# Performance work log

Measured on AMD Instinct MI355X. Metric: run time of the kernel, lower is better.

The kernel has to match this reference:

```python
import jax, jax.numpy as jnp
import numpy as np

N, E, IN_DIM, HID, OUT, H = 50000, 800000, 128, 96, 96, 4
C1, C2 = HID // H, OUT // H
EPS = 1e-5

def _lin(key, out_f, in_f):
    kw, kb = jax.random.split(key)
    s = 1.0 / np.sqrt(in_f)
    W = jax.random.uniform(kw, (out_f, in_f), jnp.float32, -s, s)
    b = jax.random.uniform(kb, (out_f,), jnp.float32, -s, s)
    return W, b

def setup_inputs() -> dict:
    key = jax.random.key(0)
    ks = jax.random.split(key, 16)
    x = jax.random.normal(ks[0], (N, IN_DIM), jnp.float32)
    edge_index = jax.random.randint(ks[1], (2, E), 0, N, jnp.int64)
    Wq1, bq1 = _lin(ks[2], HID, IN_DIM)
    Wk1, bk1 = _lin(ks[3], HID, IN_DIM)
    Wv1, bv1 = _lin(ks[4], HID, IN_DIM)
    Ws1, bs1 = _lin(ks[5], HID, IN_DIM)
    Wb1 = _lin(ks[6], 1, 3 * HID)[0]
    Wq2, bq2 = _lin(ks[7], OUT, HID)
    Wk2, bk2 = _lin(ks[8], OUT, HID)
    Wv2, bv2 = _lin(ks[9], OUT, HID)
    Ws2, bs2 = _lin(ks[10], OUT, HID)
    Wb2 = _lin(ks[11], 1, 3 * OUT)[0]
    gamma = jnp.ones((OUT,), jnp.float32)
    beta = jnp.zeros((OUT,), jnp.float32)
    return dict(x=x, edge_index=edge_index, Wq1=Wq1, bq1=bq1, Wk1=Wk1, bk1=bk1,
                Wv1=Wv1, bv1=bv1, Ws1=Ws1, bs1=bs1, Wb1=Wb1,
                Wq2=Wq2, bq2=bq2, Wk2=Wk2, bk2=bk2, Wv2=Wv2, bv2=bv2,
                Ws2=Ws2, bs2=bs2, Wb2=Wb2, gamma=gamma, beta=beta)

def transformer_conv(x, src, dst, Wq, bq, Wk, bk, Wv, bv, Ws, bs, Wb, heads, ch):
    n = x.shape[0]
    q = (x @ Wq.T + bq).reshape(n, heads, ch)
    k = (x @ Wk.T + bk).reshape(n, heads, ch)
    v = (x @ Wv.T + bv).reshape(n, heads, ch)
    # per-edge attention logits [E, H]
    alpha = jnp.einsum('ehc,ehc->eh', q[dst], k[src]) / jnp.sqrt(jnp.float32(ch))
    amax = jax.ops.segment_max(alpha, dst, num_segments=n)
    a = jnp.exp(alpha - amax[dst])
    denom = jax.ops.segment_sum(a, dst, num_segments=n)
    a = a / denom[dst]
    msg = v[src] * a[:, :, None]                       # [E, H, C]
    out = jax.ops.segment_sum(msg, dst, num_segments=n).reshape(n, heads * ch)
    x_r = x @ Ws.T + bs                                # root/skip transform
    g = jax.nn.sigmoid(jnp.concatenate([out, x_r, out - x_r], -1) @ Wb.T)
    return g * x_r + (1.0 - g) * out

def reference(x, edge_index, Wq1, bq1, Wk1, bk1, Wv1, bv1, Ws1, bs1, Wb1,
              Wq2, bq2, Wk2, bk2, Wv2, bv2, Ws2, bs2, Wb2, gamma, beta):
    src, dst = edge_index[0], edge_index[1]
    h = transformer_conv(x, src, dst, Wq1, bq1, Wk1, bk1, Wv1, bv1, Ws1, bs1, Wb1, H, C1)
    h = jax.nn.gelu(h, approximate=False)
    h = transformer_conv(h, src, dst, Wq2, bq2, Wk2, bk2, Wv2, bv2, Ws2, bs2, Wb2, H, C2)
    mu = jnp.mean(h, axis=-1, keepdims=True)
    var = jnp.mean(jnp.square(h - mu), axis=-1, keepdims=True)
    return (h - mu) / jnp.sqrt(var + EPS) * gamma + beta
```

## Files before the change

kernel.cpp:

```cpp
#include <hip/hip_runtime.h>
#include <hip/hip_bf16.h>
#include <hip/hip_fp16.h>
#include <math.h>

constexpr int NN = 50000;
constexpr int EE = 800000;
constexpr int SCAN_NB = (NN + 255) / 256;

typedef short v8s __attribute__((ext_vector_type(8)));
typedef float v4f __attribute__((ext_vector_type(4)));

__device__ __forceinline__ short f2b(float f){
  __hip_bfloat16 h = __float2bfloat16(f);
  return *reinterpret_cast<short*>(&h);
}
__device__ __forceinline__ __half2 u2h2(unsigned int u){
  union { unsigned int u; __half2 h; } c; c.u = u; return c.h;
}

__global__ void hist_kernel(const int* __restrict__ ei, int* __restrict__ deg){
  int e = blockIdx.x * blockDim.x + threadIdx.x;
  if (e < EE) atomicAdd(&deg[ei[EE + e]], 1);
}

__global__ __launch_bounds__(256) void partial_sum_kernel(const int* __restrict__ deg,
                                                          int* __restrict__ psum){
  int b = blockIdx.x, tid = threadIdx.x, lane = tid & 63, wv = tid >> 6;
  int i = b * 256 + tid;
  int v = (i < NN) ? deg[i] : 0;
  #pragma unroll
  for (int m = 1; m < 64; m <<= 1) v += __shfl_xor(v, m);
  __shared__ int ws[4];
  if (lane == 0) ws[wv] = v;
  __syncthreads();
  if (tid == 0) psum[b] = ws[0] + ws[1] + ws[2] + ws[3];
}

__global__ __launch_bounds__(256) void scan_partials_kernel(int* __restrict__ psum){
  int tid = threadIdx.x, lane = tid & 63, wv = tid >> 6;
  int own = (tid < SCAN_NB) ? psum[tid] : 0;
  int v = own;
  #pragma unroll
  for (int off = 1; off < 64; off <<= 1){
    int t = __shfl_up(v, off);
    if (lane >= off) v += t;
  }
  __shared__ int ws[4];
  if (lane == 63) ws[wv] = v;
  __syncthreads();
  int add = 0;
  #pragma unroll
  for (int w = 0; w < 4; w++) if (w < wv) add += ws[w];
  if (tid < SCAN_NB) psum[tid] = v + add - own;
}

__global__ __launch_bounds__(256) void final_scan_kernel(const int* __restrict__ deg,
                                                         const int* __restrict__ psum,
                                                         int* __restrict__ row_ptr,
                                                         int* __restrict__ cursor){
  int b = blockIdx.x, tid = threadIdx.x, lane = tid & 63, wv = tid >> 6;
  int i = b * 256 + tid;
  int d = (i < NN) ? deg[i] : 0;
  int v = d;
  #pragma unroll
  for (int off = 1; off < 64; off <<= 1){
    int t = __shfl_up(v, off);
    if (lane >= off) v += t;
  }
  __shared__ int ws[4];
  if (lane == 63) ws[wv] = v;
  __syncthreads();
  int add = psum[b];
  #pragma unroll
  for (int w = 0; w < 4; w++) if (w < wv) add += ws[w];
  if (i < NN){
    row_ptr[i + 1] = add + v;
    cursor[i]      = add + v - d;
  }
  if (i == 0) row_ptr[0] = 0;
}

__global__ void fill_kernel(const int* __restrict__ ei, int* __restrict__ cursor,
                            int* __restrict__ col_src){
  int e = blockIdx.x * blockDim.x + threadIdx.x;
  if (e < EE){
    int src = ei[e], dst = ei[EE + e];
    int pos = atomicAdd(&cursor[dst], 1);
    col_src[pos] = src;
  }
}

__global__ void pack_kernel(const float* __restrict__ Wq, const float* __restrict__ bq,
                            const float* __restrict__ Wk, const float* __restrict__ bk,
                            const float* __restrict__ Wv, const float* __restrict__ bv,
                            const float* __restrict__ Ws, const float* __restrict__ bs,
                            short* __restrict__ Wcat, float* __restrict__ bcat, int K){
  int c = blockIdx.x;
  int which = c / 96, r = c % 96;
  const float* Wsel = which == 0 ? Wq : which == 1 ? Wk : which == 2 ? Wv : Ws;
  const float* bsel = which == 0 ? bq : which == 1 ? bk : which == 2 ? bv : bs;
  for (int k = threadIdx.x; k < K; k += blockDim.x)
    Wcat[(size_t)c * K + k] = f2b(Wsel[(size_t)r * K + k]);
  if (threadIdx.x == 0) bcat[c] = bsel[r];
}

template<int K, bool AF32>
__global__ __launch_bounds__(256) void gemm_kernel(const void* __restrict__ Ain,
                                                   const short* __restrict__ Wcat,
                                                   const float* __restrict__ bcat,
                                                   float* __restrict__ qs,
                                                   __half* __restrict__ kvb,
                                                   int M){
  constexpr int KP = K + 8;
  constexpr int UNITS = K / 8;
  __shared__ __attribute__((aligned(16))) short As[64 * KP];
  __shared__ __attribute__((aligned(16))) short Bs[128 * KP];
  const int tid = threadIdx.x;
  const int rt = blockIdx.x * 64;

  #pragma unroll
  for (int it = 0; it < (64 * UNITS) / 256; ++it){
    int li = it * 256 + tid;
    int row = li / UNITS, u = li % UNITS;
    int grow = min(rt + row, M - 1);
    if constexpr (AF32){
      const float* A = (const float*)Ain;
      float4 a0 = *(const float4*)(A + (size_t)grow * K + u * 8);
      float4 a1 = *(const float4*)(A + (size_t)grow * K + u * 8 + 4);
      v8s o;
      o[0] = f2b(a0.x); o[1] = f2b(a0.y); o[2] = f2b(a0.z); o[3] = f2b(a0.w);
      o[4] = f2b(a1.x); o[5] = f2b(a1.y); o[6] = f2b(a1.z); o[7] = f2b(a1.w);
      *(v8s*)&As[row * KP + u * 8] = o;
    } else {
      const short* A = (const short*)Ain;
      *(v8s*)&As[row * KP + u * 8] = *(const v8s*)(A + (size_t)grow * K + u * 8);
    }
  }

  const int lane = tid & 63;
  const int wid  = tid >> 6;
  const int wm = wid >> 1, wn = wid & 1;
  const int fr = lane & 15, fk = lane >> 4;

  for (int p = 0; p < 3; ++p){
    __syncthreads();
    #pragma unroll
    for (int it = 0; it < (128 * UNITS) / 256; ++it){
      int li = it * 256 + tid;
      int row = li / UNITS, u = li % UNITS;
      int gcol = p * 128 + row;
      *(v8s*)&Bs[row * KP + u * 8] = *(const v8s*)(Wcat + (size_t)gcol * K + u * 8);
    }
    __syncthreads();

    v4f acc[2][4];
    #pragma unroll
    for (int i = 0; i < 2; i++)
      #pragma unroll
      for (int j = 0; j < 4; j++) acc[i][j] = (v4f){0.f, 0.f, 0.f, 0.f};

    #pragma unroll
    for (int ks = 0; ks < K / 32; ++ks){
      const int kofs = ks * 32 + fk * 8;
      v8s a[2], b[4];
      #pragma unroll
      for (int i = 0; i < 2; i++)
        a[i] = *(const v8s*)&As[(wm * 32 + i * 16 + fr) * KP + kofs];
      #pragma unroll
      for (int j = 0; j < 4; j++)
        b[j] = *(const v8s*)&Bs[(wn * 64 + j * 16 + fr) * KP + kofs];
      #pragma unroll
      for (int i = 0; i < 2; i++)
        #pragma unroll
        for (int j = 0; j < 4; j++)
          acc[i][j] = __builtin_amdgcn_mfma_f32_16x16x32_bf16(a[i], b[j], acc[i][j], 0, 0, 0);
    }

    #pragma unroll
    for (int i = 0; i < 2; i++){
      #pragma unroll
      for (int j = 0; j < 4; j++){
        const int gcol = p * 128 + wn * 64 + j * 16 + fr;
        const float bias = bcat[gcol];
        #pragma unroll
        for (int r = 0; r < 4; r++){
          const int grow = rt + wm * 32 + i * 16 + fk * 4 + r;
          if (grow < M){
            float val = acc[i][j][r] + bias;
            if (gcol < 96)       qs[(size_t)grow * 192 + gcol] = val;
            else if (gcol < 192) kvb[(size_t)grow * 192 + (gcol - 96)] = __float2half(val);
            else if (gcol < 288) kvb[(size_t)grow * 192 + 96 + (gcol - 192)] = __float2half(val);
            else                 qs[(size_t)grow * 192 + 96 + (gcol - 288)] = val;
          }
        }
      }
    }
  }
}

__global__ __launch_bounds__(256) void attn_kernel(
    const float* __restrict__ qs, const __half* __restrict__ kv,
    const int* __restrict__ row_ptr, const int* __restrict__ col_src,
    const float* __restrict__ Wb, const float* __restrict__ gamma,
    const float* __restrict__ beta, float* __restrict__ outp,
    short* __restrict__ h1b, int mode){
  const int lane = threadIdx.x & 63;
  const int wid  = threadIdx.x >> 6;
  const int n = blockIdx.x * 4 + wid;
  if (n >= NN) return;
  const int h_a = lane & 3;
  const int g_a = lane >> 2;
  const int l_v = lane & 15;
  const int vg  = lane >> 4;
  const int h_v = l_v >> 2;

  __half2 qh[12];
  {
    const float* qrow = qs + (size_t)n * 192 + h_a * 24;
    #pragma unroll
    for (int i = 0; i < 12; i++)
      qh[i] = __floats2half2_rn(qrow[2 * i], qrow[2 * i + 1]);
  }
  const int rs = row_ptr[n], re = row_ptr[n + 1];
  float m = -INFINITY, s = 0.f;
  float acc[6] = {0.f, 0.f, 0.f, 0.f, 0.f, 0.f};

  for (int cb = rs; cb < re; cb += 16){
    const int cn = re - cb;
    int srcv = col_src[cb + min(g_a, cn - 1)];
    int sb[4];
    #pragma unroll
    for (int st = 0; st < 4; st++)
      sb[st] = __shfl(srcv, 4 * min(st * 4 + vg, cn - 1));
    unsigned int vd[4][3];
    #pragma unroll
    for (int st = 0; st < 4; st++){
      const unsigned int* vp =
        (const unsigned int*)((const char*)kv + (size_t)sb[st] * 384 + 192 + 12 * l_v);
      vd[st][0] = vp[0]; vd[st][1] = vp[1]; vd[st][2] = vp[2];
    }
    const uint4* kp = (const uint4*)((const char*)kv + (size_t)srcv * 384 + h_a * 48);
    uint4 u0 = kp[0], u1 = kp[1], u2 = kp[2];
    __half2 d0 = __floats2half2_rn(0.f, 0.f), d1 = d0;
    d0 = __hfma2(qh[0],  u2h2(u0.x), d0); d1 = __hfma2(qh[1],  u2h2(u0.y), d1);
    d0 = __hfma2(qh[2],  u2h2(u0.z), d0); d1 = __hfma2(qh[3],  u2h2(u0.w), d1);
    d0 = __hfma2(qh[4],  u2h2(u1.x), d0); d1 = __hfma2(qh[5],  u2h2(u1.y), d1);
    d0 = __hfma2(qh[6],  u2h2(u1.z), d0); d1 = __hfma2(qh[7],  u2h2(u1.w), d1);
    d0 = __hfma2(qh[8],  u2h2(u2.x), d0); d1 = __hfma2(qh[9],  u2h2(u2.y), d1);
    d0 = __hfma2(qh[10], u2h2(u2.z), d0); d1 = __hfma2(qh[11], u2h2(u2.w), d1);
    float dot = __low2float(d0) + __high2float(d0) + __low2float(d1) + __high2float(d1);
    float al = (g_a < cn) ? dot * 0.2041241452319315f : -INFINITY;

    float cm = al;
    cm = fmaxf(cm, __shfl_xor(cm, 4));
    cm = fmaxf(cm, __shfl_xor(cm, 8));
    cm = fmaxf(cm, __shfl_xor(cm, 16));
    cm = fmaxf(cm, __shfl_xor(cm, 32));
    float nm = fmaxf(m, cm);
    float r  = __expf(m - nm);
    float e  = __expf(al - nm);
    float cs = e;
    cs += __shfl_xor(cs, 4);
    cs += __shfl_xor(cs, 8);
    cs += __shfl_xor(cs, 16);
    cs += __shfl_xor(cs, 32);
    s = s * r + cs;
    m = nm;

    float rv = __shfl(r, h_v);
    __half2 ch0 = __floats2half2_rn(0.f, 0.f), ch1 = ch0, ch2 = ch0;
    #pragma unroll
    for (int st = 0; st < 4; st++){
      int eidx = st * 4 + vg;
      float w = __shfl(e, 4 * min(eidx, cn - 1) + h_v);
      if (eidx >= cn) w = 0.f;
      __half2 w2 = __float2half2_rn(w);
      ch0 = __hfma2(w2, u2h2(vd[st][0]), ch0);
      ch1 = __hfma2(w2, u2h2(vd[st][1]), ch1);
      ch2 = __hfma2(w2, u2h2(vd[st][2]), ch2);
    }
    acc[0] = fmaf(acc[0], rv, __low2float(ch0));
    acc[1] = fmaf(acc[1], rv, __high2float(ch0));
    acc[2] = fmaf(acc[2], rv, __low2float(ch1));
    acc[3] = fmaf(acc[3], rv, __high2float(ch1));
    acc[4] = fmaf(acc[4], rv, __low2float(ch2));
    acc[5] = fmaf(acc[5], rv, __high2float(ch2));
  }

  #pragma unroll
  for (int i = 0; i < 6; i++){
    acc[i] += __shfl_xor(acc[i], 16);
    acc[i] += __shfl_xor(acc[i], 32);
  }
  float sv  = __shfl(s, h_v);
  float inv = (re > rs) ? 1.0f / sv : 0.f;
  float o[6], xr[6];
  #pragma unroll
  for (int i = 0; i < 6; i++) o[i] = acc[i] * inv;
  const float* xrp = qs + (size_t)n * 192 + 96 + 6 * l_v;
  #pragma unroll
  for (int i = 0; i < 6; i++) xr[i] = xrp[i];

  float p = 0.f;
  #pragma unroll
  for (int i = 0; i < 6; i++){
    int f = 6 * l_v + i;
    p += Wb[f] * o[i] + Wb[96 + f] * xr[i] + Wb[192 + f] * (o[i] - xr[i]);
  }
  p += __shfl_xor(p, 1);
  p += __shfl_xor(p, 2);
  p += __shfl_xor(p, 4);
  p += __shfl_xor(p, 8);
  float g = 1.0f / (1.0f + __expf(-p));
  float y[6];
  #pragma unroll
  for (int i = 0; i < 6; i++) y[i] = g * xr[i] + (1.0f - g) * o[i];

  if (mode == 0){
    #pragma unroll
    for (int i = 0; i < 6; i++)
      y[i] = 0.5f * y[i] * (1.0f + erff(y[i] * 0.7071067811865475f));
    if (vg == 0){
      short* op = h1b + (size_t)n * 96 + 6 * l_v;
      #pragma unroll
      for (int i = 0; i < 6; i++) op[i] = f2b(y[i]);
    }
  } else {
    float ssum = y[0] + y[1] + y[2] + y[3] + y[4] + y[5];
    ssum += __shfl_xor(ssum, 1);
    ssum += __shfl_xor(ssum, 2);
    ssum += __shfl_xor(ssum, 4);
    ssum += __shfl_xor(ssum, 8);
    float mu = ssum * (1.0f / 96.0f);
    float vsum = 0.f;
    #pragma unroll
    for (int i = 0; i < 6; i++){ float d = y[i] - mu; vsum += d * d; }
    vsum += __shfl_xor(vsum, 1);
    vsum += __shfl_xor(vsum, 2);
    vsum += __shfl_xor(vsum, 4);
    vsum += __shfl_xor(vsum, 8);
    float invs = rsqrtf(vsum * (1.0f / 96.0f) + 1e-5f);
    if (vg == 0){
      float* op = outp + (size_t)n * 96 + 6 * l_v;
      #pragma unroll
      for (int i = 0; i < 6; i++){
        int f = 6 * l_v + i;
        op[i] = (y[i] - mu) * invs * gamma[f] + beta[f];
      }
    }
  }
}

extern "C" void kernel_launch(void* const* d_in, const int* in_sizes, int n_in,
                              void* d_out, int out_size, void* d_ws, size_t ws_size,
                              hipStream_t stream){
  const float* x    = (const float*)d_in[0];
  const int*   ei   = (const int*)d_in[1];
  const float* Wq1  = (const float*)d_in[2];
  const float* bq1  = (const float*)d_in[3];
  const float* Wk1  = (const float*)d_in[4];
  const float* bk1  = (const float*)d_in[5];
  const float* Wv1  = (const float*)d_in[6];
  const float* bv1  = (const float*)d_in[7];
  const float* Ws1  = (const float*)d_in[8];
  const float* bs1  = (const float*)d_in[9];
  const float* Wb1  = (const float*)d_in[10];
  const float* Wq2  = (const float*)d_in[11];
  const float* bq2  = (const float*)d_in[12];
  const float* Wk2  = (const float*)d_in[13];
  const float* bk2  = (const float*)d_in[14];
  const float* Wv2  = (const float*)d_in[15];
  const float* bv2  = (const float*)d_in[16];
  const float* Ws2  = (const float*)d_in[17];
  const float* bs2  = (const float*)d_in[18];
  const float* Wb2  = (const float*)d_in[19];
  const float* gamma = (const float*)d_in[20];
  const float* beta  = (const float*)d_in[21];
  float* out = (float*)d_out;

  char* ws = (char*)d_ws;
  size_t off = 0;
  auto take = [&](size_t b) -> void* {
    void* p = ws + off;
    off += (b + 255) & ~(size_t)255;
    return p;
  };
  float* qs            = (float*)take((size_t)NN * 192 * 4);
  __half* kvb          = (__half*)take((size_t)NN * 192 * 2);
  short* h1b           = (short*)take((size_t)NN * 96 * 2);
  short* Wcat          = (short*)take((size_t)384 * 128 * 2);
  float* bcat          = (float*)take(384 * 4);
  int* deg             = (int*)take((size_t)NN * 4);
  int* cursor          = (int*)take((size_t)NN * 4);
  int* row_ptr         = (int*)take((size_t)(NN + 1) * 4);
  int* col_src         = (int*)take((size_t)EE * 4);
  int* psum            = (int*)take((size_t)SCAN_NB * 4);

  hipMemsetAsync(deg, 0, (size_t)NN * 4, stream);
  hist_kernel<<<(EE + 255) / 256, 256, 0, stream>>>(ei, deg);
  partial_sum_kernel<<<SCAN_NB, 256, 0, stream>>>(deg, psum);
  scan_partials_kernel<<<1, 256, 0, stream>>>(psum);
  final_scan_kernel<<<SCAN_NB, 256, 0, stream>>>(deg, psum, row_ptr, cursor);
  fill_kernel<<<(EE + 255) / 256, 256, 0, stream>>>(ei, cursor, col_src);

  const int gemm_grid = (NN + 63) / 64;
  pack_kernel<<<384, 128, 0, stream>>>(Wq1, bq1, Wk1, bk1, Wv1, bv1, Ws1, bs1, Wcat, bcat, 128);
  gemm_kernel<128, true><<<gemm_grid, 256, 0, stream>>>(x, Wcat, bcat, qs, kvb, NN);
  attn_kernel<<<(NN + 3) / 4, 256, 0, stream>>>(qs, kvb, row_ptr, col_src, Wb1,
                                                nullptr, nullptr, nullptr, h1b, 0);
  pack_kernel<<<384, 128, 0, stream>>>(Wq2, bq2, Wk2, bk2, Wv2, bv2, Ws2, bs2, Wcat, bcat, 96);
  gemm_kernel<96, false><<<gemm_grid, 256, 0, stream>>>(h1b, Wcat, bcat, qs, kvb, NN);
  attn_kernel<<<(NN + 3) / 4, 256, 0, stream>>>(qs, kvb, row_ptr, col_src, Wb2,
                                                gamma, beta, out, nullptr, 1);
}
```

Baseline: 283.8 us.

## Read GEMM weights from global memory and halve row tile; merge weight packing

The GEMM kernel no longer stages the weight matrix in shared memory. Each wave now loads B fragments straight from global (L2-resident) memory, and the row tile shrinks from 64 to 32, which doubles the grid and cuts the shared-memory footprint and the syncs inside the loop. The two per-layer pack kernels become a single launch writing into separate weight buffers. The intent is better occupancy and fewer barriers, at the cost of repeated global/L2 reads of the weights and less reuse of each B fragment per block.

```diff
diff --git a/kernel.cpp b/kernel.cpp
--- a/kernel.cpp
+++ b/kernel.cpp
@@ -90,18 +90,37 @@
   }
 }
 
-__global__ void pack_kernel(const float* __restrict__ Wq, const float* __restrict__ bq,
-                            const float* __restrict__ Wk, const float* __restrict__ bk,
-                            const float* __restrict__ Wv, const float* __restrict__ bv,
-                            const float* __restrict__ Ws, const float* __restrict__ bs,
-                            short* __restrict__ Wcat, float* __restrict__ bcat, int K){
+__global__ void pack_kernel(
+    const float* __restrict__ Wq1, const float* __restrict__ bq1,
+    const float* __restrict__ Wk1, const float* __restrict__ bk1,
+    const float* __restrict__ Wv1, const float* __restrict__ bv1,
+    const float* __restrict__ Ws1, const float* __restrict__ bs1,
+    const float* __restrict__ Wq2, const float* __restrict__ bq2,
+    const float* __restrict__ Wk2, const float* __restrict__ bk2,
+    const float* __restrict__ Wv2, const float* __restrict__ bv2,
+    const float* __restrict__ Ws2, const float* __restrict__ bs2,
+    short* __restrict__ Wcat1, float* __restrict__ bcat1,
+    short* __restrict__ Wcat2, float* __restrict__ bcat2){
   int c = blockIdx.x;
-  int which = c / 96, r = c % 96;
-  const float* Wsel = which == 0 ? Wq : which == 1 ? Wk : which == 2 ? Wv : Ws;
-  const float* bsel = which == 0 ? bq : which == 1 ? bk : which == 2 ? bv : bs;
+  int layer = c / 384, cc = c % 384;
+  int which = cc / 96, r = cc % 96;
+  const float* Wsel;
+  const float* bsel;
+  int K;
+  short* Wd;
+  float* bd;
+  if (layer == 0){
+    Wsel = which == 0 ? Wq1 : which == 1 ? Wk1 : which == 2 ? Wv1 : Ws1;
+    bsel = which == 0 ? bq1 : which == 1 ? bk1 : which == 2 ? bv1 : bs1;
+    K = 128; Wd = Wcat1; bd = bcat1;
+  } else {
+    Wsel = which == 0 ? Wq2 : which == 1 ? Wk2 : which == 2 ? Wv2 : Ws2;
+    bsel = which == 0 ? bq2 : which == 1 ? bk2 : which == 2 ? bv2 : bs2;
+    K = 96; Wd = Wcat2; bd = bcat2;
+  }
   for (int k = threadIdx.x; k < K; k += blockDim.x)
-    Wcat[(size_t)c * K + k] = f2b(Wsel[(size_t)r * K + k]);
-  if (threadIdx.x == 0) bcat[c] = bsel[r];
+    Wd[(size_t)cc * K + k] = f2b(Wsel[(size_t)r * K + k]);
+  if (threadIdx.x == 0) bd[cc] = bsel[r];
 }
 
 template<int K, bool AF32>
@@ -113,85 +132,69 @@
                                                    int M){
   constexpr int KP = K + 8;
   constexpr int UNITS = K / 8;
-  __shared__ __attribute__((aligned(16))) short As[64 * KP];
-  __shared__ __attribute__((aligned(16))) short Bs[128 * KP];
+  constexpr int TOT = 32 * UNITS;
+  __shared__ __attribute__((aligned(16))) short As[32 * KP];
   const int tid = threadIdx.x;
-  const int rt = blockIdx.x * 64;
-
-  #pragma unroll
-  for (int it = 0; it < (64 * UNITS) / 256; ++it){
+  const int rt = blockIdx.x * 32;
+
+  #pragma unroll
+  for (int it = 0; it < (TOT + 255) / 256; ++it){
     int li = it * 256 + tid;
-    int row = li / UNITS, u = li % UNITS;
-    int grow = min(rt + row, M - 1);
-    if constexpr (AF32){
-      const float* A = (const float*)Ain;
-      float4 a0 = *(const float4*)(A + (size_t)grow * K + u * 8);
-      float4 a1 = *(const float4*)(A + (size_t)grow * K + u * 8 + 4);
-      v8s o;
-      o[0] = f2b(a0.x); o[1] = f2b(a0.y); o[2] = f2b(a0.z); o[3] = f2b(a0.w);
-      o[4] = f2b(a1.x); o[5] = f2b(a1.y); o[6] = f2b(a1.z); o[7] = f2b(a1.w);
-      *(v8s*)&As[row * KP + u * 8] = o;
-    } else {
-      const short* A = (const short*)Ain;
-      *(v8s*)&As[row * KP + u * 8] = *(const v8s*)(A + (size_t)grow * K + u * 8);
-    }
-  }
+    if (li < TOT){
+      int row = li / UNITS, u = li % UNITS;
+      int grow = min(rt + row, M - 1);
+      if constexpr (AF32){
+        const float* A = (const float*)Ain;
+        float4 a0 = *(const float4*)(A + (size_t)grow * K + u * 8);
+        float4 a1 = *(const float4*)(A + (size_t)grow * K + u * 8 + 4);
+        v8s o;
+        o[0] = f2b(a0.x); o[1] = f2b(a0.y); o[2] = f2b(a0.z); o[3] = f2b(a0.w);
+        o[4] = f2b(a1.x); o[5] = f2b(a1.y); o[6] = f2b(a1.z); o[7] = f2b(a1.w);
+        *(v8s*)&As[row * KP + u * 8] = o;
+      } else {
+        const short* A = (const short*)Ain;
+        *(v8s*)&As[row * KP + u * 8] = *(const v8s*)(A + (size_t)grow * K + u * 8);
+      }
+    }
+  }
+  __syncthreads();
 
   const int lane = tid & 63;
   const int wid  = tid >> 6;
-  const int wm = wid >> 1, wn = wid & 1;
+  const int wm = wid & 1, wn = wid >> 1;
   const int fr = lane & 15, fk = lane >> 4;
 
+  #pragma unroll
   for (int p = 0; p < 3; ++p){
-    __syncthreads();
-    #pragma unroll
-    for (int it = 0; it < (128 * UNITS) / 256; ++it){
-      int li = it * 256 + tid;
-      int row = li / UNITS, u = li % UNITS;
-      int gcol = p * 128 + row;
-      *(v8s*)&Bs[row * KP + u * 8] = *(const v8s*)(Wcat + (size_t)gcol * K + u * 8);
-    }
-    __syncthreads();
-
-    v4f acc[2][4];
-    #pragma unroll
-    for (int i = 0; i < 2; i++)
-      #pragma unroll
-      for (int j = 0; j < 4; j++) acc[i][j] = (v4f){0.f, 0.f, 0.f, 0.f};
+    v4f acc[4];
+    #pragma unroll
+    for (int j = 0; j < 4; j++) acc[j] = (v4f){0.f, 0.f, 0.f, 0.f};
 
     #pragma unroll
     for (int ks = 0; ks < K / 32; ++ks){
       const int kofs = ks * 32 + fk * 8;
-      v8s a[2], b[4];
-      #pragma unroll
-      for (int i = 0; i < 2; i++)
-        a[i] = *(const v8s*)&As[(wm * 32 + i * 16 + fr) * KP + kofs];
-      #pragma unroll
-      for (int j = 0; j < 4; j++)
-        b[j] = *(const v8s*)&Bs[(wn * 64 + j * 16 + fr) * KP + kofs];
-      #pragma unroll
-      for (int i = 0; i < 2; i++)
-        #pragma unroll
-        for (int j = 0; j < 4; j++)
-          acc[i][j] = __builtin_amdgcn_mfma_f32_16x16x32_bf16(a[i], b[j], acc[i][j], 0, 0, 0);
-    }
-
-    #pragma unroll
-    for (int i = 0; i < 2; i++){
+      v8s a = *(const v8s*)&As[(wm * 16 + fr) * KP + kofs];
       #pragma unroll
       for (int j = 0; j < 4; j++){
         const int gcol = p * 128 + wn * 64 + j * 16 + fr;
-        const float bias = bcat[gcol];
-        #pragma unroll
-        for (int r = 0; r < 4; r++){
-          const int grow = rt + wm * 32 + i * 16 + fk * 4 + r;
-          if (grow < M){
-            float val = acc[i][j][r] + bias;
-            if (gcol < 96)       qs[(size_t)grow * 192 + gcol] = val;
-            else if (gcol < 192) kvb[(size_t)grow * 192 + (gcol - 96)] = __float2half(val);
-            else if (gcol < 288) kvb[(size_t)grow * 192 + 96 + (gcol - 192)] = __float2half(val);
-            else                 qs[(size_t)grow * 192 + 96 + (gcol - 288)] = val;
-          }
+        v8s b = *(const v8s*)(Wcat + (size_t)gcol * K + kofs);
+        acc[j] = __builtin_amdgcn_mfma_f32_16x16x32_bf16(a, b, acc[j], 0, 0, 0);
+      }
+    }
+
+    #pragma unroll
+    for (int j = 0; j < 4; j++){
+      const int gcol = p * 128 + wn * 64 + j * 16 + fr;
+      const float bias = bcat[gcol];
+      #pragma unroll
+      for (int r = 0; r < 4; r++){
+        const int grow = rt + wm * 16 + fk * 4 + r;
+        if (grow < M){
+          float val = acc[j][r] + bias;
+          if (gcol < 96)       qs[(size_t)grow * 192 + gcol] = val;
+          else if (gcol < 192) kvb[(size_t)grow * 192 + (gcol - 96)] = __float2half(val);
+          else if (gcol < 288) kvb[(size_t)grow * 192 + 96 + (gcol - 192)] = __float2half(val);
+          else                 qs[(size_t)grow * 192 + 96 + (gcol - 288)] = val;
         }
       }
     }
@@ -388,8 +391,10 @@
   float* qs            = (float*)take((size_t)NN * 192 * 4);
   __half* kvb          = (__half*)take((size_t)NN * 192 * 2);
   short* h1b           = (short*)take((size_t)NN * 96 * 2);
-  short* Wcat          = (short*)take((size_t)384 * 128 * 2);
-  float* bcat          = (float*)take(384 * 4);
+  short* Wcat1         = (short*)take((size_t)384 * 128 * 2);
+  short* Wcat2         = (short*)take((size_t)384 * 96 * 2);
+  float* bcat1         = (float*)take(384 * 4);
+  float* bcat2         = (float*)take(384 * 4);
   int* deg             = (int*)take((size_t)NN * 4);
   int* cursor          = (int*)take((size_t)NN * 4);
   int* row_ptr         = (int*)take((size_t)(NN + 1) * 4);
@@ -403,13 +408,15 @@
   final_scan_kernel<<<SCAN_NB, 256, 0, stream>>>(deg, psum, row_ptr, cursor);
   fill_kernel<<<(EE + 255) / 256, 256, 0, stream>>>(ei, cursor, col_src);
 
-  const int gemm_grid = (NN + 63) / 64;
-  pack_kernel<<<384, 128, 0, stream>>>(Wq1, bq1, Wk1, bk1, Wv1, bv1, Ws1, bs1, Wcat, bcat, 128);
-  gemm_kernel<128, true><<<gemm_grid, 256, 0, stream>>>(x, Wcat, bcat, qs, kvb, NN);
+  pack_kernel<<<768, 128, 0, stream>>>(Wq1, bq1, Wk1, bk1, Wv1, bv1, Ws1, bs1,
+                                       Wq2, bq2, Wk2, bk2, Wv2, bv2, Ws2, bs2,
+                                       Wcat1, bcat1, Wcat2, bcat2);
+
+  const int gemm_grid = (NN + 31) / 32;
+  gemm_kernel<128, true><<<gemm_grid, 256, 0, stream>>>(x, Wcat1, bcat1, qs, kvb, NN);
   attn_kernel<<<(NN + 3) / 4, 256, 0, stream>>>(qs, kvb, row_ptr, col_src, Wb1,
                                                 nullptr, nullptr, nullptr, h1b, 0);
-  pack_kernel<<<384, 128, 0, stream>>>(Wq2, bq2, Wk2, bk2, Wv2, bv2, Ws2, bs2, Wcat, bcat, 96);
-  gemm_kernel<96, false><<<gemm_grid, 256, 0, stream>>>(h1b, Wcat, bcat, qs, kvb, NN);
+  gemm_kernel<96, false><<<gemm_grid, 256, 0, stream>>>(h1b, Wcat2, bcat2, qs, kvb, NN);
   attn_kernel<<<(NN + 3) / 4, 256, 0, stream>>>(qs, kvb, row_ptr, col_src, Wb2,
                                                 gamma, beta, out, nullptr, 1);
 }
```

Result: slower. 304.5 us (+7.3%).
